# Performance work log

Hardware: AMD Instinct MI355X
Metric: run time of the kernel (lower is better)

## Reference

```python
import jax, jax.numpy as jnp
import numpy as np

N = 50000          # nodes
E = 1_600_000      # edges
R = 16             # num_relations
NB = 4             # num_bases
FIN = 128          # num_node_features
H = 128            # hidden_channels
G = 64             # num graphs in batch
NC = 2             # num_classes


def rgcn_conv(x, edge_index, edge_type, bases, comp, root, bias):
    """PyG RGCNConv with basis decomposition, mean aggregation per relation."""
    n = x.shape[0]
    # weight[r] = sum_b comp[r,b] * bases[b]  -> [R, in, out]
    weight = jnp.einsum('rb,bio->rio', comp, bases)
    src, dst = edge_index[0], edge_index[1]
    # segment id combining destination node and relation
    seg = dst * R + edge_type                      # [E]
    msg = x[src]                                   # [E, in] gather
    summed = jax.ops.segment_sum(msg, seg, num_segments=n * R)      # [N*R, in]
    cnt = jax.ops.segment_sum(jnp.ones((msg.shape[0],), x.dtype), seg,
                              num_segments=n * R)                   # [N*R]
    mean = summed / jnp.maximum(cnt, 1.0)[:, None]
    mean = mean.reshape(n, R, -1)                  # [N, R, in]
    out = jnp.einsum('nri,rio->no', mean, weight) + x @ root + bias
    return out


def global_mean_pool(x, batch, num_graphs):
    s = jax.ops.segment_sum(x, batch, num_segments=num_graphs)
    c = jax.ops.segment_sum(jnp.ones((x.shape[0],), x.dtype), batch,
                            num_segments=num_graphs)
    return s / jnp.maximum(c, 1.0)[:, None]


def setup_inputs() -> dict:
    key = jax.random.key(0)
    ks = jax.random.split(key, 24)
    inp = {
        'x': jax.random.normal(ks[0], (N, FIN), jnp.float32),
        'edge_index': jax.random.randint(ks[1], (2, E), 0, N),
        'edge_type': jax.random.randint(ks[2], (E,), 0, R),
        'batch': jnp.sort(jax.random.randint(ks[3], (N,), 0, G)),
        'rel_labels': jax.random.randint(ks[4], (G,), 0, R),
        'drop_prob': 0,
        'rel_emb': jax.random.normal(ks[5], (R, H), jnp.float32),
    }
    s1 = 1.0 / np.sqrt(FIN)
    s2 = 1.0 / np.sqrt(H)
    inp['bases1'] = jax.random.normal(ks[6], (NB, FIN, H), jnp.float32) * s1
    inp['comp1'] = jax.random.normal(ks[7], (R, NB), jnp.float32)
    inp['root1'] = jax.random.normal(ks[8], (FIN, H), jnp.float32) * s1
    inp['bias1'] = jnp.zeros((H,), jnp.float32)
    inp['bases2'] = jax.random.normal(ks[9], (NB, H, H), jnp.float32) * s2
    inp['comp2'] = jax.random.normal(ks[10], (R, NB), jnp.float32)
    inp['root2'] = jax.random.normal(ks[11], (H, H), jnp.float32) * s2
    inp['bias2'] = jnp.zeros((H,), jnp.float32)
    inp['bases3'] = jax.random.normal(ks[12], (NB, H, H), jnp.float32) * s2
    inp['comp3'] = jax.random.normal(ks[13], (R, NB), jnp.float32)
    inp['root3'] = jax.random.normal(ks[14], (H, H), jnp.float32) * s2
    inp['bias3'] = jnp.zeros((H,), jnp.float32)
    inp['lin_w'] = jax.random.normal(ks[15], (2 * H, NC), jnp.float32) * (1.0 / np.sqrt(2 * H))
    inp['lin_b'] = jnp.zeros((NC,), jnp.float32)
    return inp


def reference(x, edge_index, edge_type, batch, rel_labels, drop_prob, rel_emb,
              bases1, comp1, root1, bias1,
              bases2, comp2, root2, bias2,
              bases3, comp3, root3, bias3,
              lin_w, lin_b):
    rel_embs = rel_emb[rel_labels]                               # [G, H]
    h = jax.nn.relu(rgcn_conv(x, edge_index, edge_type, bases1, comp1, root1, bias1))
    h = jax.nn.relu(rgcn_conv(h, edge_index, edge_type, bases2, comp2, root2, bias2))
    h = rgcn_conv(h, edge_index, edge_type, bases3, comp3, root3, bias3)
    pooled = global_mean_pool(h, batch, G)                       # [G, H]
    z = jnp.concatenate([pooled, rel_embs], axis=1)              # [G, 2H]
    # dropout with p=drop_prob in eval mode (reference is deterministic) -> identity
    return z @ lin_w + lin_b                                     # [G, NC]
```

## Files before the change

kernel.cpp:

```cpp
#include <hip/hip_runtime.h>

#define NN 50000
#define EE 1600000
#define RR 16
#define NBASE 4
#define FINF 128
#define HD 128
#define NG 64
#define NCLS 2
#define NRSEG (NN*RR)

typedef __attribute__((ext_vector_type(8))) short short8;
typedef __attribute__((ext_vector_type(4))) float f32x4;
typedef __attribute__((ext_vector_type(2))) float f32x2;
typedef unsigned short u16;
typedef unsigned int u32;
typedef unsigned long long u64;
typedef unsigned char u8;

__device__ __forceinline__ float bflo(u32 u){ return __builtin_bit_cast(float, u << 16); }
__device__ __forceinline__ float bfhi(u32 u){ return __builtin_bit_cast(float, u & 0xFFFF0000u); }
__device__ __forceinline__ u16 f2bf(float f){
  u32 u = __builtin_bit_cast(u32, f);
  u += 0x7FFFu + ((u >> 16) & 1u);
  return (u16)(u >> 16);
}
__device__ __forceinline__ u32 pack2(float a, float b){
  return (u32)f2bf(a) | ((u32)f2bf(b) << 16);
}
__device__ __forceinline__ u32 cvt_pk_bf16(float a, float b){
  u32 r;
  asm("v_cvt_pk_bf16_f32 %0, %1, %2" : "=v"(r) : "v"(a), "v"(b));
  return r;
}
__device__ __forceinline__ float fastrcp(float x){
#if __has_builtin(__builtin_amdgcn_rcpf)
  return __builtin_amdgcn_rcpf(x);
#else
  return 1.0f / x;
#endif
}
__device__ __forceinline__ float ldf(const void* p, int i, int isbf){
  return isbf ? bflo((u32)((const u16*)p)[i]) : ((const float*)p)[i];
}

__device__ __forceinline__ float fp8_manual(u32 b){
  u32 s = (b>>7)&1, e = (b>>3)&15, m = b&7;
  float v;
  if (e==0) v = (float)m * 0.001953125f;
  else      v = __builtin_bit_cast(float, ((e+120u)<<23) | (m<<20));
  return s ? -v : v;
}
__device__ __forceinline__ u32 f32_to_fp8_manual(float f){
  u32 u = __builtin_bit_cast(u32, f);
  u32 s = u>>31;
  int e = (int)((u>>23)&0xFF);
  u32 m = u & 0x7FFFFF;
  int ee = e - 120;
  if (ee <= 0) return s<<7;
  u32 m3 = m >> 20, rem = m & 0xFFFFF;
  u32 rnd = (rem > 0x80000u) || (rem == 0x80000u && (m3 & 1));
  m3 += rnd;
  if (m3 == 8){ m3 = 0; ee += 1; }
  if (ee >= 16){ ee = 15; m3 = 6; }
  return (s<<7) | ((u32)ee<<3) | m3;
}
__device__ __forceinline__ void fp8x2_to_f32(u32 v, float& a, float& b){
#if __has_builtin(__builtin_amdgcn_cvt_pk_f32_fp8)
  f32x2 r = __builtin_amdgcn_cvt_pk_f32_fp8((int)v, false);
  a = r[0]; b = r[1];
#else
  a = fp8_manual(v & 0xFF); b = fp8_manual((v>>8)&0xFF);
#endif
}
__device__ __forceinline__ u32 pk_fp8x2(float a, float b){
  a = fminf(fmaxf(a, -448.f), 448.f);
  b = fminf(fmaxf(b, -448.f), 448.f);
#if __has_builtin(__builtin_amdgcn_cvt_pk_fp8_f32)
  return (u32)__builtin_amdgcn_cvt_pk_fp8_f32(a, b, 0, false) & 0xFFFF;
#else
  return f32_to_fp8_manual(a) | (f32_to_fp8_manual(b) << 8);
#endif
}

__global__ void k_detect(const u32* __restrict__ xw, int* __restrict__ flag){
  __shared__ int votes;
  if (threadIdx.x == 0) votes = 0;
  __syncthreads();
  u32 w = xw[threadIdx.x];
  int e = (w >> 7) & 0xFF;
  if (e >= 100 && e <= 129) atomicAdd(&votes, 1);
  __syncthreads();
  if (threadIdx.x == 0) flag[0] = (votes >= 192) ? 1 : 0;
}

__global__ void k_quant(const void* __restrict__ src, u8* __restrict__ dstq,
                        const int* __restrict__ flagp, int* __restrict__ cnt){
  int i = blockIdx.x*256 + threadIdx.x;
  if (i < NRSEG) cnt[i] = 0;
  if (i >= NN*HD/4) return;
  int isbf = flagp[0];
  float v0,v1,v2,v3;
  if (isbf){
    u32 a = ((const u32*)src)[i*2+0], b = ((const u32*)src)[i*2+1];
    v0=bflo(a); v1=bfhi(a); v2=bflo(b); v3=bfhi(b);
  } else {
    float4 f = ((const float4*)src)[i];
    v0=f.x; v1=f.y; v2=f.z; v3=f.w;
  }
  u32 q = pk_fp8x2(v0,v1) | (pk_fp8x2(v2,v3) << 16);
  ((u32*)dstq)[i] = q;
}


__global__ void k_hist(const int* __restrict__ dst, const int* __restrict__ et,
                       int* __restrict__ cnt){
  int e = blockIdx.x*256 + threadIdx.x;
  if (e < EE) atomicAdd(&cnt[et[e]*NN + dst[e]], 1);
}

#define SCB 1024
__global__ __launch_bounds__(SCB) void k_scan1(const int* __restrict__ cnt,
                                               int* __restrict__ off,
                                               int* __restrict__ bsum){
  __shared__ int sh[SCB];
  int tid = threadIdx.x;
  int i = blockIdx.x*SCB + tid;
  int v = (i < NRSEG) ? cnt[i] : 0;
  sh[tid] = v; __syncthreads();
  for (int d=1; d<SCB; d<<=1){
    int t = (tid >= d) ? sh[tid-d] : 0;
    __syncthreads();
    sh[tid] += t;
    __syncthreads();
  }
  if (i < NRSEG) off[i] = sh[tid] - v;
  if (tid == SCB-1) bsum[blockIdx.x] = sh[SCB-1];
}

__global__ __launch_bounds__(1024) void k_scan2(int* __restrict__ bsum, int nb){
  __shared__ int sh[1024];
  __shared__ int carry;
  int tid = threadIdx.x;
  if (tid == 0) carry = 0;
  __syncthreads();
  for (int base=0; base<nb; base+=1024){
    int i = base + tid;
    int v = (i < nb) ? bsum[i] : 0;
    int orig = v;
    sh[tid] = v; __syncthreads();
    for (int d=1; d<1024; d<<=1){
      int t = (tid >= d) ? sh[tid-d] : 0;
      __syncthreads();
      sh[tid] += t;
      __syncthreads();
    }
    int total = sh[1023];
    int excl = sh[tid] - orig + carry;
    if (i < nb) bsum[i] = excl;
    __syncthreads();
    if (tid == 0) carry += total;
    __syncthreads();
  }
}

__global__ __launch_bounds__(SCB) void k_scan3(const int* __restrict__ cnt,
                                               int* __restrict__ off,
                                               const int* __restrict__ bsum){
  int i = blockIdx.x*SCB + threadIdx.x;
  if (i < NRSEG){
    int o = off[i] + bsum[blockIdx.x];
    off[i] = o;
    if (i == NRSEG-1) off[NRSEG] = o + cnt[i];
  }
}

__global__ void k_scatter(const int* __restrict__ src, const int* __restrict__ dst,
                          const int* __restrict__ et, const int* __restrict__ off,
                          int* __restrict__ cnt, int* __restrict__ esrc){
  int e = blockIdx.x*256 + threadIdx.x;
  if (e < EE){
    int seg = et[e]*NN + dst[e];
    int p = atomicSub(&cnt[seg], 1) - 1;
    esrc[off[seg] + p] = src[e];
  }
}


__global__ void k_weights3(const void* __restrict__ b0, const void* __restrict__ c0,
                           const void* __restrict__ r0,
                           const void* __restrict__ b1, const void* __restrict__ c1,
                           const void* __restrict__ r1,
                           const void* __restrict__ b2, const void* __restrict__ c2,
                           const void* __restrict__ r2,
                           u16* __restrict__ WTf, const int* __restrict__ flagp){
  int gid = blockIdx.x;
  int layer = gid / 1088;
  int blk = gid - layer*1088;
  int idx = blk*256 + threadIdx.x;
  if (idx >= 17*16384) return;
  const void* bases = (layer==0) ? b0 : (layer==1) ? b1 : b2;
  const void* comp  = (layer==0) ? c0 : (layer==1) ? c1 : c2;
  const void* root  = (layer==0) ? r0 : (layer==1) ? r1 : r2;
  u16* W = WTf + (u32)layer * (17*16384);
  int isbf = flagp[0];
  int r = idx >> 14;
  int o = (idx >> 7) & 127;
  int i = idx & 127;
  float v;
  if (r < RR){
    v = 0.f;
    #pragma unroll
    for (int b=0;b<NBASE;b++)
      v += ldf(comp, r*NBASE+b, isbf) * ldf(bases, (b*FINF + i)*HD + o, isbf);
  } else {
    v = ldf(root, i*HD + o, isbf);
  }
  int wv = o >> 5, ct = (o >> 4) & 1, mrow = o & 15;
  int ks = i >> 5, quad = (i >> 3) & 3, j = i & 7;
  int lane = quad*16 + mrow;
  W[(u32)((((r*4+wv)*2+ct)*4+ks)*64 + lane)*8 + j] = f2bf(v);
}


#define TN 16

__global__ __launch_bounds__(256, 6) void k_layer(
    const u8*  __restrict__ xq,
    const u16* __restrict__ WTf,
    const void* __restrict__ bias, const int* __restrict__ off,
    const int* __restrict__ esrc,
    u16* __restrict__ hout,
    u8* __restrict__ hq,
    const int* __restrict__ flagp, int write_bf, int relu)
{
  __shared__ __align__(16) u16 Abuf[4][TN*136];
  __shared__ int soff[RR*17];
  int tid = threadIdx.x;
  int n0 = blockIdx.x * TN;
  int isbf_in = flagp[0];

  int wv = tid >> 6;
  int lane = tid & 63;
  int lane2 = lane << 1;
  int mrow = lane & 15;
  int quad = lane >> 4;

  for (int i = tid; i < RR*17; i += 256){
    int r = i / 17, k = i - r*17;
    soff[i] = off[r*NN + n0 + k];
  }
  __syncthreads();

  f32x4 acc[2];
  { f32x4 z = {0.f,0.f,0.f,0.f}; acc[0] = z; acc[1] = z; }

  for (int t=0; t<4; ++t){
    int r = t*4 + wv;
    {
      int offv = 0;
      if (lane <= 16) offv = soff[r*17 + lane];
      int wstart = __builtin_amdgcn_readlane(offv, 0);
      int wend   = __builtin_amdgcn_readlane(offv, 16);
      int blen = wend - wstart;

      float a0 = 0.f, a1 = 0.f;
      int idx = 0;
      int cb = wstart;
      int nb = __builtin_amdgcn_readlane(offv, 1);
      u16* abase = Abuf[wv] + lane*2;

      auto doflush = [&](){
        int cnt = nb - cb;
        float cf = (float)(cnt > 0 ? cnt : 1);
        float inv = fastrcp(cf);
        *(u32*)(abase + idx*136) = cvt_pk_bf16(a0*inv, a1*inv);
        a0 = 0.f; a1 = 0.f;
        cb = nb; idx++;
        if (idx < TN) nb = __builtin_amdgcn_readlane(offv, idx+1);
      };
      auto consume = [&](int ae, u32 w){
        while (idx < TN && nb <= ae) doflush();
        float da, db; fp8x2_to_f32(w, da, db);
        a0 += da; a1 += db;
      };

      if (blen > 0 && blen <= 128){
        int ei0 = esrc[wstart + (lane < blen ? lane : 0)];
        int ei1 = (blen > 64) ? esrc[wstart + 64 + (lane < blen-64 ? lane : 0)] : 0;

        auto section = [&](int eiv, int sbeg, int L){
          u32 wa[8], wb[8];
          #pragma unroll
          for (int k=0;k<8;k++){
            int ee = k < L ? k : L-1;
            int sid = __builtin_amdgcn_readlane(eiv, ee);
            wa[k] = (u32)*(const u16*)(xq + ((u64)(u32)sid << 7) + lane2);
          }
          for (int b0 = 0; b0 < L; b0 += 16){
            if (b0 + 8 < L){
              #pragma unroll
              for (int k=0;k<8;k++){
                int e2 = b0+8+k; int ee = e2 < L ? e2 : L-1;
                int sid = __builtin_amdgcn_readlane(eiv, ee);
                wb[k] = (u32)*(const u16*)(xq + ((u64)(u32)sid << 7) + lane2);
              }
            }
            #pragma unroll
            for (int k=0;k<8;k++){
              int e = b0 + k;
              if (e < L) consume(sbeg + e, wa[k]);
            }
            if (b0 + 16 < L){
              #pragma unroll
              for (int k=0;k<8;k++){
                int e2 = b0+16+k; int ee = e2 < L ? e2 : L-1;
                int sid = __builtin_amdgcn_readlane(eiv, ee);
                wa[k] = (u32)*(const u16*)(xq + ((u64)(u32)sid << 7) + lane2);
              }
            }
            #pragma unroll
            for (int k=0;k<8;k++){
              int e = b0 + 8 + k;
              if (e < L) consume(sbeg + e, wb[k]);
            }
          }
        };
        int L0 = blen < 64 ? blen : 64;
        section(ei0, wstart, L0);
        if (blen > 64) section(ei1, wstart + 64, blen - 64);
      } else if (blen > 0){
        for (int e = wstart; e < wend; ++e){
          int sid = __builtin_amdgcn_readfirstlane(esrc[e]);
          consume(e, (u32)*(const u16*)(xq + ((u64)(u32)sid << 7) + lane2));
        }
      }
      while (idx < TN) doflush();
    }
    __syncthreads();
    #pragma unroll
    for (int rloc=0; rloc<4; ++rloc){
      int rr = t*4 + rloc;
      const u16* Bp = WTf + (u32)(((rr*4 + wv)*2)*4*64)*8 + (u32)lane*8;
      #pragma unroll
      for (int ks=0; ks<4; ++ks){
        short8 af = *(const short8*)(Abuf[rloc] + mrow*136 + ks*32 + quad*8);
        #pragma unroll
        for (int ct=0; ct<2; ++ct){
          short8 bf = *(const short8*)(Bp + (u32)(ct*4 + ks)*64*8);
          acc[ct] = __builtin_amdgcn_mfma_f32_16x16x32_bf16(af, bf, acc[ct], 0, 0, 0);
        }
      }
    }
    __syncthreads();
  }
  {
    const u8* xrow = xq + (u32)(n0 + mrow)*HD;
    const u16* Bp = WTf + (u32)(((16*4 + wv)*2)*4*64)*8 + (u32)lane*8;
    #pragma unroll
    for (int ks=0; ks<4; ++ks){
      u32 lo = *(const u32*)(xrow + ks*32 + quad*8);
      u32 hi = *(const u32*)(xrow + ks*32 + quad*8 + 4);
      float f0,f1,f2,f3,f4,f5,f6,f7;
      fp8x2_to_f32(lo & 0xFFFFu, f0, f1);
      fp8x2_to_f32(lo >> 16,     f2, f3);
      fp8x2_to_f32(hi & 0xFFFFu, f4, f5);
      fp8x2_to_f32(hi >> 16,     f6, f7);
      union { short8 v; u32 w[4]; } u;
      u.w[0] = cvt_pk_bf16(f0,f1); u.w[1] = cvt_pk_bf16(f2,f3);
      u.w[2] = cvt_pk_bf16(f4,f5); u.w[3] = cvt_pk_bf16(f6,f7);
      #pragma unroll
      for (int ct=0; ct<2; ++ct){
        short8 bf = *(const short8*)(Bp + (u32)(ct*4 + ks)*64*8);
        acc[ct] = __builtin_amdgcn_mfma_f32_16x16x32_bf16(u.v, bf, acc[ct], 0, 0, 0);
      }
    }
  }
  #pragma unroll
  for (int ct=0; ct<2; ++ct){
    int col = wv*32 + ct*16 + mrow;
    float bv = ldf(bias, col, isbf_in);
    #pragma unroll
    for (int rg=0; rg<4; ++rg){
      int n = n0 + quad*4 + rg;
      float v = acc[ct][rg] + bv;
      if (relu) v = fmaxf(v, 0.f);
      if (!(v == v)) v = 0.f;
      if (write_bf) hout[(u32)(n*HD + col)] = f2bf(v);
      else          hq[(u32)(n*HD + col)] = (u8)(pk_fp8x2(v, 0.f) & 0xFF);
    }
  }
}


__global__ __launch_bounds__(1024) void k_pool_head(
    const u16* __restrict__ h, const int* __restrict__ batch,
    const int* __restrict__ rlab, const void* __restrict__ rel_emb,
    const void* __restrict__ lin_w, const void* __restrict__ lin_b,
    void* __restrict__ out, const int* __restrict__ flagp)
{
  int g = blockIdx.x;
  int isbf = flagp[0];
  __shared__ int bounds[2];
  __shared__ float psum[8][128];
  __shared__ float red[4];
  if (threadIdx.x == 0){
    int lo=0, hi=NN;
    while (lo < hi){ int m=(lo+hi)>>1; if (batch[m] < g) lo=m+1; else hi=m; }
    bounds[0] = lo;
    int lo2=lo, hi2=NN;
    while (lo2 < hi2){ int m=(lo2+hi2)>>1; if (batch[m] < g+1) lo2=m+1; else hi2=m; }
    bounds[1] = lo2;
  }
  __syncthreads();
  int lo = bounds[0], hi = bounds[1];
  int f = threadIdx.x & 127;
  int s = threadIdx.x >> 7;
  float acc = 0.f;
  for (int n = lo + s; n < hi; n += 8) acc += bflo((u32)h[(u32)(n*HD + f)]);
  psum[s][f] = acc;
  __syncthreads();
  if (threadIdx.x < 128){
    int cn = hi - lo;
    float tot = 0.f;
    #pragma unroll
    for (int k=0;k<8;k++) tot += psum[k][f];
    float pooled = tot / (float)(cn > 0 ? cn : 1);
    int rl = rlab[g];
    float re = ldf(rel_emb, rl*HD + f, isbf);
    float v0 = pooled * ldf(lin_w, f*NCLS+0, isbf) + re * ldf(lin_w, (HD+f)*NCLS+0, isbf);
    float v1 = pooled * ldf(lin_w, f*NCLS+1, isbf) + re * ldf(lin_w, (HD+f)*NCLS+1, isbf);
    #pragma unroll
    for (int o=32;o>0;o>>=1){ v0 += __shfl_down(v0,o); v1 += __shfl_down(v1,o); }
    int ln = threadIdx.x & 63, wvv = threadIdx.x >> 6;
    if (ln == 0){ red[wvv*2] = v0; red[wvv*2+1] = v1; }
  }
  __syncthreads();
  if (threadIdx.x == 0){
    float o0 = red[0] + red[2] + ldf(lin_b, 0, isbf);
    float o1 = red[1] + red[3] + ldf(lin_b, 1, isbf);
    if (isbf){
      ((u16*)out)[g*NCLS+0] = f2bf(o0);
      ((u16*)out)[g*NCLS+1] = f2bf(o1);
    } else {
      ((float*)out)[g*NCLS+0] = o0;
      ((float*)out)[g*NCLS+1] = o1;
    }
  }
}


extern "C" void kernel_launch(void* const* d_in, const int* in_sizes, int n_in,
                              void* d_out, int out_size, void* d_ws, size_t ws_size,
                              hipStream_t stream)
{
  (void)in_sizes; (void)n_in; (void)out_size; (void)ws_size;
  const void* x      = d_in[0];
  const int* eidx    = (const int*)d_in[1];
  const int* etype   = (const int*)d_in[2];
  const int* batch   = (const int*)d_in[3];
  const int* rlab    = (const int*)d_in[4];
  const void* rel_emb = d_in[6];
  const void* basesA[3] = {d_in[7],  d_in[11], d_in[15]};
  const void* compA[3]  = {d_in[8],  d_in[12], d_in[16]};
  const void* rootA[3]  = {d_in[9],  d_in[13], d_in[17]};
  const void* biasA[3]  = {d_in[10], d_in[14], d_in[18]};
  const void* lin_w  = d_in[19];
  const void* lin_b  = d_in[20];

  char* p = (char*)d_ws;
  auto alloc = [&](size_t bytes)->char*{ char* r = p; p += (bytes + 255) & ~(size_t)255; return r; };
  int*   flag   = (int*)  alloc(256);
  int*   off    = (int*)  alloc((size_t)(NRSEG+1)*4);
  int*   esrc   = (int*)  alloc((size_t)(EE+64)*4);
  u16*   WTf    = (u16*)  alloc((size_t)3*17*16384*2);
  u8*    xq     = (u8*)   alloc((size_t)NN*HD);
  u8*    h1q    = (u8*)   alloc((size_t)NN*HD);
  u8*    h2q    = (u8*)   alloc((size_t)NN*HD);
  u16*   h3     = (u16*)  alloc((size_t)NN*HD*2);
  int*   cnt    = (int*)h3;
  int*   bsum   = (int*)((char*)h3 + (size_t)NRSEG*4);

  const int* src_in = eidx;
  const int* dst_in = eidx + EE;

  const int nscan = (NRSEG + SCB - 1) / SCB;

  k_detect <<<1, 256, 0, stream>>>((const u32*)x, flag);
  k_quant  <<<(NN*HD/4 + 255)/256, 256, 0, stream>>>(x, xq, flag, cnt);
  k_hist   <<<EE/256, 256, 0, stream>>>(dst_in, etype, cnt);
  k_scan1  <<<nscan, SCB, 0, stream>>>(cnt, off, bsum);
  k_scan2  <<<1,    1024, 0, stream>>>(bsum, nscan);
  k_scan3  <<<nscan, SCB, 0, stream>>>(cnt, off, bsum);
  k_scatter<<<EE/256, 256, 0, stream>>>(src_in, dst_in, etype, off, cnt, esrc);

  k_weights3<<<3*1088, 256, 0, stream>>>(basesA[0], compA[0], rootA[0],
                                         basesA[1], compA[1], rootA[1],
                                         basesA[2], compA[2], rootA[2],
                                         WTf, flag);

  const int nblk = NN / TN;
  u16* W0 = WTf;
  u16* W1 = WTf + (size_t)1*17*16384;
  u16* W2 = WTf + (size_t)2*17*16384;
  k_layer<<<nblk, 256, 0, stream>>>(xq,  W0, biasA[0], off, esrc, (u16*)0, h1q, flag, 0, 1);
  k_layer<<<nblk, 256, 0, stream>>>(h1q, W1, biasA[1], off, esrc, (u16*)0, h2q, flag, 0, 1);
  k_layer<<<nblk, 256, 0, stream>>>(h2q, W2, biasA[2], off, esrc, h3, (u8*)0, flag, 1, 0);

  k_pool_head<<<NG, 1024, 0, stream>>>(h3, batch, rlab, rel_emb, lin_w, lin_b,
                                       d_out, flag);
}
```

Before: 643.3 us.

## Stage neighbor row gathers into LDS via async DMA overlapped with MFMA

Replaces the per-edge global loads of fp8 neighbor rows with global_load_lds DMA transfers into a per-wave LDS buffer of up to 64 edges. The next relation's edge rows are prefetched while the current block runs its MFMA stage, and longer segments are handled in chunks. The goal is to hide gather latency and issue wider 16-byte transfers. The extra LDS cuts launch-bounds occupancy from 6 to 3 blocks, and the added vmcnt waits may serialize work.

```diff
diff --git a/kernel.cpp b/kernel.cpp
--- a/kernel.cpp
+++ b/kernel.cpp
@@ -42,6 +42,10 @@
 }
 __device__ __forceinline__ float ldf(const void* p, int i, int isbf){
   return isbf ? bflo((u32)((const u16*)p)[i]) : ((const float*)p)[i];
+}
+__device__ __forceinline__ void dma16(const u8* g, u8* l){
+  __builtin_amdgcn_global_load_lds((const __attribute__((address_space(1))) u32*)g,
+                                   (__attribute__((address_space(3))) u32*)l, 16, 0, 0);
 }
 
 __device__ __forceinline__ float fp8_manual(u32 b){
@@ -224,8 +228,9 @@
 
 
 #define TN 16
-
-__global__ __launch_bounds__(256, 6) void k_layer(
+#define ECHUNK 64
+
+__global__ __launch_bounds__(256, 3) void k_layer(
     const u8*  __restrict__ xq,
     const u16* __restrict__ WTf,
     const void* __restrict__ bias, const int* __restrict__ off,
@@ -236,15 +241,16 @@
 {
   __shared__ __align__(16) u16 Abuf[4][TN*136];
   __shared__ int soff[RR*17];
+  __shared__ __align__(16) u8 Ebuf[4][ECHUNK*HD];
   int tid = threadIdx.x;
   int n0 = blockIdx.x * TN;
   int isbf_in = flagp[0];
 
   int wv = tid >> 6;
   int lane = tid & 63;
-  int lane2 = lane << 1;
   int mrow = lane & 15;
   int quad = lane >> 4;
+  int lo16 = (lane & 7) << 4;
 
   for (int i = tid; i < RR*17; i += 256){
     int r = i / 17, k = i - r*17;
@@ -255,19 +261,61 @@
   f32x4 acc[2];
   { f32x4 z = {0.f,0.f,0.f,0.f}; acc[0] = z; acc[1] = z; }
 
+  auto load_eids = [&](int ws, int bl, u32* eid){
+    int blc = bl < ECHUNK ? bl : ECHUNK;
+    int nfull = (blc + 7) >> 3;
+    #pragma unroll
+    for (int k=0;k<8;k++){
+      if (k < nfull){
+        int q = k*8 + (lane >> 3);
+        q = q < bl ? q : bl-1;
+        eid[k] = (u32)esrc[ws + q];
+      }
+    }
+  };
+  auto issue_dma = [&](const u32* eid, int bl){
+    int blc = bl < ECHUNK ? bl : ECHUNK;
+    int nfull = (blc + 7) >> 3;
+    u8* lb = (u8*)Ebuf[wv];
+    #pragma unroll
+    for (int k=0;k<8;k++){
+      if (k < nfull){
+        const u8* gp = xq + ((u64)eid[k] << 7) + lo16;
+        dma16(gp, lb + k*1024);
+      }
+    }
+  };
+
+  int offvC = (lane <= 16) ? soff[wv*17 + lane] : 0;
+  int wsC = __builtin_amdgcn_readlane(offvC, 0);
+  int blC = __builtin_amdgcn_readlane(offvC, 16) - wsC;
+  if (blC > 0){
+    u32 eid0[8];
+    load_eids(wsC, blC, eid0);
+    issue_dma(eid0, blC);
+  }
+
   for (int t=0; t<4; ++t){
-    int r = t*4 + wv;
+    asm volatile("s_waitcnt vmcnt(0)" ::: "memory");
+    __builtin_amdgcn_sched_barrier(0);
+
+    int offvN = 0, wsN = 0, blN = 0;
+    u32 eidN[8];
+    #pragma unroll
+    for (int k=0;k<8;k++) eidN[k] = 0;
+    if (t < 3){
+      int rn = (t+1)*4 + wv;
+      offvN = (lane <= 16) ? soff[rn*17 + lane] : 0;
+      wsN = __builtin_amdgcn_readlane(offvN, 0);
+      blN = __builtin_amdgcn_readlane(offvN, 16) - wsN;
+      if (blN > 0) load_eids(wsN, blN, eidN);
+    }
+
     {
-      int offv = 0;
-      if (lane <= 16) offv = soff[r*17 + lane];
-      int wstart = __builtin_amdgcn_readlane(offv, 0);
-      int wend   = __builtin_amdgcn_readlane(offv, 16);
-      int blen = wend - wstart;
-
+      int idx = 0;
+      int cb = wsC;
+      int nb = __builtin_amdgcn_readlane(offvC, 1);
       float a0 = 0.f, a1 = 0.f;
-      int idx = 0;
-      int cb = wstart;
-      int nb = __builtin_amdgcn_readlane(offv, 1);
       u16* abase = Abuf[wv] + lane*2;
 
       auto doflush = [&](){
@@ -277,67 +325,50 @@
         *(u32*)(abase + idx*136) = cvt_pk_bf16(a0*inv, a1*inv);
         a0 = 0.f; a1 = 0.f;
         cb = nb; idx++;
-        if (idx < TN) nb = __builtin_amdgcn_readlane(offv, idx+1);
+        if (idx < TN) nb = __builtin_amdgcn_readlane(offvC, idx+1);
       };
-      auto consume = [&](int ae, u32 w){
-        while (idx < TN && nb <= ae) doflush();
-        float da, db; fp8x2_to_f32(w, da, db);
-        a0 += da; a1 += db;
-      };
-
-      if (blen > 0 && blen <= 128){
-        int ei0 = esrc[wstart + (lane < blen ? lane : 0)];
-        int ei1 = (blen > 64) ? esrc[wstart + 64 + (lane < blen-64 ? lane : 0)] : 0;
-
-        auto section = [&](int eiv, int sbeg, int L){
-          u32 wa[8], wb[8];
+      auto accum_chunk = [&](int abeg, int aend, int lbase){
+        const u16* Eb = (const u16*)Ebuf[wv];
+        for (int b0 = abeg; b0 < aend; b0 += 16){
+          u32 w[16];
           #pragma unroll
-          for (int k=0;k<8;k++){
-            int ee = k < L ? k : L-1;
-            int sid = __builtin_amdgcn_readlane(eiv, ee);
-            wa[k] = (u32)*(const u16*)(xq + ((u64)(u32)sid << 7) + lane2);
+          for (int k=0;k<16;k++){
+            int ee = b0 + k; ee = ee < aend ? ee : aend-1;
+            w[k] = (u32)Eb[(u32)(ee - lbase)*64 + lane];
           }
-          for (int b0 = 0; b0 < L; b0 += 16){
-            if (b0 + 8 < L){
-              #pragma unroll
-              for (int k=0;k<8;k++){
-                int e2 = b0+8+k; int ee = e2 < L ? e2 : L-1;
-                int sid = __builtin_amdgcn_readlane(eiv, ee);
-                wb[k] = (u32)*(const u16*)(xq + ((u64)(u32)sid << 7) + lane2);
-              }
-            }
-            #pragma unroll
-            for (int k=0;k<8;k++){
-              int e = b0 + k;
-              if (e < L) consume(sbeg + e, wa[k]);
-            }
-            if (b0 + 16 < L){
-              #pragma unroll
-              for (int k=0;k<8;k++){
-                int e2 = b0+16+k; int ee = e2 < L ? e2 : L-1;
-                int sid = __builtin_amdgcn_readlane(eiv, ee);
-                wa[k] = (u32)*(const u16*)(xq + ((u64)(u32)sid << 7) + lane2);
-              }
-            }
-            #pragma unroll
-            for (int k=0;k<8;k++){
-              int e = b0 + 8 + k;
-              if (e < L) consume(sbeg + e, wb[k]);
+          #pragma unroll
+          for (int k=0;k<16;k++){
+            int e = b0 + k;
+            if (e < aend){
+              while (idx < TN && nb <= e) doflush();
+              float da, db; fp8x2_to_f32(w[k], da, db);
+              a0 += da; a1 += db;
             }
           }
-        };
-        int L0 = blen < 64 ? blen : 64;
-        section(ei0, wstart, L0);
-        if (blen > 64) section(ei1, wstart + 64, blen - 64);
-      } else if (blen > 0){
-        for (int e = wstart; e < wend; ++e){
-          int sid = __builtin_amdgcn_readfirstlane(esrc[e]);
-          consume(e, (u32)*(const u16*)(xq + ((u64)(u32)sid << 7) + lane2));
         }
+      };
+
+      int c0 = blC < ECHUNK ? blC : ECHUNK;
+      if (c0 > 0) accum_chunk(wsC, wsC + c0, wsC);
+      for (int ch = ECHUNK; ch < blC; ch += ECHUNK){
+        asm volatile("s_waitcnt lgkmcnt(0)" ::: "memory");
+        __builtin_amdgcn_sched_barrier(0);
+        int cl = blC - ch; if (cl > ECHUNK) cl = ECHUNK;
+        u32 eidS[8];
+        #pragma unroll
+        for (int k=0;k<8;k++) eidS[k] = 0;
+        load_eids(wsC + ch, cl, eidS);
+        issue_dma(eidS, cl);
+        asm volatile("s_waitcnt vmcnt(0)" ::: "memory");
+        __builtin_amdgcn_sched_barrier(0);
+        accum_chunk(wsC + ch, wsC + ch + cl, wsC + ch);
       }
       while (idx < TN) doflush();
     }
     __syncthreads();
+
+    if (t < 3 && blN > 0) issue_dma(eidN, blN);
+
     #pragma unroll
     for (int rloc=0; rloc<4; ++rloc){
       int rr = t*4 + rloc;
@@ -353,6 +384,8 @@
       }
     }
     __syncthreads();
+
+    offvC = offvN; wsC = wsN; blC = blN;
   }
   {
     const u8* xrow = xq + (u32)(n0 + mrow)*HD;
```

Result: slower. 740.8 us (+15.1%).
